# Optimization experiments

Measured on AMD Instinct MI355X. Metric: run time of the kernel, lower is better.

Reference implementation:

```python
import jax, jax.numpy as jnp
import numpy as np

N = 131072
IN_A = 256
IN_V = 512
IN_VF = 512
CH = 256
BN_EPS = 1e-5
COS_EPS = 1e-8


def setup_inputs() -> dict:
    key = jax.random.key(0)
    ks = jax.random.split(key, 12)
    s = 0.05
    return {
        "x": jax.random.normal(ks[0], (N, 4, 512), dtype=jnp.float32),
        "audio_node_mask": jax.random.bernoulli(ks[1], 0.5, (N,)),
        "W_a": jax.random.normal(ks[2], (IN_A, CH), dtype=jnp.float32) * s,
        "b_a": jnp.zeros((CH,), jnp.float32),
        "W_v": jax.random.normal(ks[3], (IN_V, CH), dtype=jnp.float32) * s,
        "b_v": jnp.zeros((CH,), jnp.float32),
        "W_f": jax.random.normal(ks[4], (2 * CH, CH), dtype=jnp.float32) * s,
        "b_f": jnp.zeros((CH,), jnp.float32),
        "gamma": jnp.ones((CH,), jnp.float32),
        "beta": jnp.zeros((CH,), jnp.float32),
        "W_fc": jax.random.normal(ks[5], (CH, 2), dtype=jnp.float32) * s,
        "b_fc": jnp.zeros((2,), jnp.float32),
    }


def reference(x, audio_node_mask, W_a, b_a, W_v, b_v, W_f, b_f, gamma, beta, W_fc, b_fc):
    # Slice per-type features (x: [N, 4, 512])
    a_in = x[:, 0, :IN_A]    # audio feats (also video->audio feats)
    v_in = x[:, 1, :IN_V]    # video feats
    a_vf = x[:, 2, :IN_VF]   # audio voice-face emb
    v_vf = x[:, 3, :IN_VF]   # video voice-face emb

    # cosine similarity along feature dim (torch.nn.functional.cosine_similarity semantics)
    dot = jnp.sum(a_vf * v_vf, axis=1)
    denom = jnp.maximum(jnp.linalg.norm(a_vf, axis=1) * jnp.linalg.norm(v_vf, axis=1), COS_EPS)
    sim = dot / denom  # [N]

    # per-type linears (compute densely, select by mask -> same math as masked scatter)
    a_out = a_in @ W_a + b_a                                   # [N, CH]
    v_out = v_in @ W_v + b_v                                   # [N, CH]
    va = a_in * sim[:, None]                                   # sim-weighted audio feats on video nodes
    fused = jnp.concatenate([va, v_out], axis=1) @ W_f + b_f   # [N, CH]

    graph_feats = jnp.where(audio_node_mask[:, None], a_out, fused)

    # BatchNorm1d (training: batch statistics, biased variance)
    mu = jnp.mean(graph_feats, axis=0)
    var = jnp.mean(jnp.square(graph_feats - mu), axis=0)
    graph_feats = (graph_feats - mu) * jax.lax.rsqrt(var + BN_EPS) * gamma + beta

    graph_feats = jax.nn.relu(graph_feats)
    return graph_feats @ W_fc + b_fc  # [N, 2]
```

## Files before the change

### kernel.cpp

```cpp
#include <hip/hip_runtime.h>
#include <hip/hip_bf16.h>
#include <stdint.h>

#define NN 131072

typedef unsigned int uint;
typedef unsigned short ushort;
typedef __attribute__((ext_vector_type(8))) __bf16 bf16x8;
typedef __attribute__((ext_vector_type(2))) __bf16 bf16x2;
typedef __attribute__((ext_vector_type(4))) float f32x4;


__device__ __forceinline__ ushort f2bf(float f) {
    uint u = __float_as_uint(f);
    u += 0x7FFF + ((u >> 16) & 1);
    return (ushort)(u >> 16);
}
__device__ __forceinline__ uint pk2(float a, float b) {
    bf16x2 t;
    t[0] = (__bf16)a;
    t[1] = (__bf16)b;
    return __builtin_bit_cast(uint, t);
}
__device__ __forceinline__ bool mask_val(const unsigned char* m8, int flag, int i) {
    return flag ? (m8[(size_t)i * 4] != 0) : (m8[i] != 0);
}
__device__ __forceinline__ size_t pack_off(int k, int c) {
    return (size_t)(((k >> 5) * 16 + (c >> 4)) * 512
                    + (((k >> 3) & 3) * 16 + (c & 15)) * 8 + (k & 7));
}

__global__ void k_detect(const uint* m32, int n, int* flag) {
    __shared__ int cnt;
    if (threadIdx.x == 0) cnt = 0;
    __syncthreads();
    int local = 0;
    int nw = n >> 2;
    for (int i = threadIdx.x; i < nw; i += 1024)
        if (m32[i] & 0x0000FF00u) local = 1;
    if (local) atomicAdd(&cnt, 1);
    __syncthreads();
    if (threadIdx.x == 0) *flag = (cnt == 0) ? 1 : 0;
}

__global__ void k_count(const unsigned char* m8, const int* flagp, int* cntM) {
    int flag = *flagp;
    int t = threadIdx.x;
    bool m = mask_val(m8, flag, blockIdx.x * 256 + t);
    unsigned long long bal = __ballot(m);
    __shared__ int wsum[4];
    if ((t & 63) == 0) wsum[t >> 6] = __popcll(bal);
    __syncthreads();
    if (t == 0) cntM[blockIdx.x] = wsum[0] + wsum[1] + wsum[2] + wsum[3];
}

__global__ void k_scan(const int* __restrict__ cntM, int* __restrict__ meta,
                       int* __restrict__ baseA, int* __restrict__ baseF) {
    __shared__ int sA[512], sF[512];
    int t = threadIdx.x;
    int a = cntM[t], f = 256 - a;
    sA[t] = a; sF[t] = f;
    __syncthreads();
    for (int off = 1; off < 512; off <<= 1) {
        int va = (t >= off) ? sA[t - off] : 0;
        int vf = (t >= off) ? sF[t - off] : 0;
        __syncthreads();
        sA[t] += va; sF[t] += vf;
        __syncthreads();
    }
    baseA[t] = sA[t] - a;
    baseF[t] = sF[t] - f;
    if (t == 511) { meta[2] = sA[511]; meta[1] = sF[511]; }
}

__global__ void k_fill(const unsigned char* m8, const int* flagp,
                       const int* __restrict__ baseA, const int* __restrict__ baseF,
                       int* __restrict__ audioIdx, int* __restrict__ fusedIdx) {
    int flag = *flagp;
    int blk = blockIdx.x, t = threadIdx.x;
    int row = blk * 256 + t;
    bool m = mask_val(m8, flag, row);
    unsigned long long bal = __ballot(m);
    int lane = t & 63, w = t >> 6;
    unsigned long long lt = (1ull << lane) - 1ull;
    int pA = __popcll(bal & lt);
    __shared__ int wA[4];
    if (lane == 0) wA[w] = __popcll(bal);
    __syncthreads();
    int offA = 0;
    for (int i = 0; i < w; ++i) offA += wA[i];
    int offF = w * 64 - offA;
    int pF = lane - pA;
    if (m) audioIdx[baseA[blk] + offA + pA] = row;
    else   fusedIdx[baseF[blk] + offF + pF] = row;
}

__global__ void k_prep(const float* __restrict__ Wa, const float* __restrict__ Wf,
                       const float* __restrict__ Wv, const float* __restrict__ bv,
                       const float* __restrict__ bf_, ushort* __restrict__ Bwa,
                       ushort* __restrict__ Bwf, float* __restrict__ cf) {
    int c = threadIdx.x;
    int b = blockIdx.x;
    if (b < 256) {
        Bwa[pack_off(b, c)] = f2bf(Wa[b * 256 + c]);
    } else if (b < 512) {
        Bwf[pack_off(512 + (b - 256), c)] = f2bf(Wf[(b - 256) * 256 + c]);
    } else if (b < 1024) {
        int k = b - 512;
        const float* wr = Wv + k * 256;
        float acc = 0.f;
        for (int j = 0; j < 256; ++j) acc += wr[j] * Wf[(256 + j) * 256 + c];
        Bwf[pack_off(k, c)] = f2bf(acc);
    } else {
        float acc = bf_[c];
        for (int j = 0; j < 256; ++j) acc += bv[j] * Wf[(256 + j) * 256 + c];
        cf[c] = acc;
    }
}

__global__ __launch_bounds__(512, 4) void k_main(
    const float* __restrict__ x, const int* __restrict__ meta,
    const int* __restrict__ fusedIdx, const int* __restrict__ audioIdx,
    const ushort* __restrict__ Bwa, const ushort* __restrict__ Bwf,
    const float* __restrict__ ba, const float* __restrict__ cf,
    ushort* __restrict__ gf, float* __restrict__ bn_s, float* __restrict__ bn_q)
{
    __shared__ bf16x8 As8[2][128 * 8];
    __shared__ int ridxS[128];
    __shared__ float simS[128];
    __shared__ unsigned char validS[128];
    __shared__ float redS[256], redQ[256];

    const int tid = threadIdx.x;
    const int cntF = meta[1], cntA = meta[2];
    const int nbF = (cntF + 127) >> 7;
    const int nbA = (cntA + 127) >> 7;
    const int b = blockIdx.x;
    const bool isF = b < nbF;
    const int bb = isF ? b : b - nbF;

    if (!isF && bb >= nbA) {
        if (tid < 256) {
            bn_s[(size_t)b * 256 + tid] = 0.f;
            bn_q[(size_t)b * 256 + tid] = 0.f;
        }
        return;
    }

    const int cnt = isF ? cntF : cntA;
    const int* idxArr = isF ? fusedIdx : audioIdx;
    const int lane = tid & 63;
    const int w = tid >> 6, wr = w >> 2, wc = w & 3;
    const int fr = lane & 15, fg = lane >> 4;

    if (tid < 128) {
        int gpos = bb * 128 + tid;
        int ok = gpos < cnt;
        ridxS[tid] = ok ? idxArr[gpos] : 0;
        validS[tid] = ok;
        simS[tid] = 1.f;
    }
    __syncthreads();

    const int NS = isF ? 12 : 4;
    const int sr = tid >> 2, sk = tid & 3;
    const float* xrow = x + (size_t)ridxS[sr] * 2048;
    const float sVf = validS[sr] ? 1.f : 0.f;
    float sAf = 0.f;

    int4 pA[2];
    auto loadA = [&](int st) {
        const float scl = (isF && st >= 8) ? sAf : sVf;
        const int off = isF ? ((st < 8) ? 512 + st * 64 : (st - 8) * 64) : st * 64;
        const float4* src = (const float4*)(xrow + off + sk * 16);
        #pragma unroll
        for (int s = 0; s < 2; ++s) {
            float4 u0 = src[2 * s], u1 = src[2 * s + 1];
            int4 p;
            p.x = pk2(u0.x * scl, u0.y * scl);
            p.y = pk2(u0.z * scl, u0.w * scl);
            p.z = pk2(u1.x * scl, u1.y * scl);
            p.w = pk2(u1.z * scl, u1.w * scl);
            pA[s] = p;
        }
    };
    auto storeA = [&](int buf) {
        #pragma unroll
        for (int s = 0; s < 2; ++s)
            As8[buf][sr * 8 + ((sk * 2 + s) ^ (sr & 7))] = __builtin_bit_cast(bf16x8, pA[s]);
    };

    loadA(0);

    if (isF) {
        #pragma unroll 2
        for (int rr = 0; rr < 16; ++rr) {
            int r = w * 16 + rr;
            const float4* p = (const float4*)(x + (size_t)ridxS[r] * 2048 + 1024);
            float4 a0 = p[lane], a1 = p[lane + 64];
            float4 v0 = p[lane + 128], v1 = p[lane + 192];
            float dot = a0.x * v0.x + a0.y * v0.y + a0.z * v0.z + a0.w * v0.w
                      + a1.x * v1.x + a1.y * v1.y + a1.z * v1.z + a1.w * v1.w;
            float na = a0.x * a0.x + a0.y * a0.y + a0.z * a0.z + a0.w * a0.w
                     + a1.x * a1.x + a1.y * a1.y + a1.z * a1.z + a1.w * a1.w;
            float nv = v0.x * v0.x + v0.y * v0.y + v0.z * v0.z + v0.w * v0.w
                     + v1.x * v1.x + v1.y * v1.y + v1.z * v1.z + v1.w * v1.w;
            #pragma unroll
            for (int off = 32; off; off >>= 1) {
                dot += __shfl_xor(dot, off);
                na  += __shfl_xor(na,  off);
                nv  += __shfl_xor(nv,  off);
            }
            if (lane == 0)
                simS[r] = dot / fmaxf(sqrtf(na) * sqrtf(nv), 1e-8f);
        }
    }
    __syncthreads();
    sAf = validS[sr] ? simS[sr] : 0.f;

    const ushort* bBase = (isF ? Bwf : Bwa) + ((size_t)(wc * 4) << 9) + (lane << 3);

    f32x4 acc[4][4];
    #pragma unroll
    for (int m = 0; m < 4; ++m)
        #pragma unroll
        for (int n = 0; n < 4; ++n) acc[m][n] = (f32x4){0.f, 0.f, 0.f, 0.f};

    storeA(0);
    __syncthreads();

    for (int st = 0; st < NS; ++st) {
        if (st + 1 < NS) loadA(st + 1);
        const int buf = st & 1;
        #pragma unroll
        for (int kk = 0; kk < 2; ++kk) {
            bf16x8 bv[4], af[4];
            #pragma unroll
            for (int n = 0; n < 4; ++n)
                bv[n] = *(const bf16x8*)(bBase + ((size_t)((st * 2 + kk) * 16 + n) << 9));
            #pragma unroll
            for (int m = 0; m < 4; ++m) {
                int r = wr * 64 + m * 16 + fr;
                af[m] = As8[buf][r * 8 + ((kk * 4 + fg) ^ (r & 7))];
            }
            #pragma unroll
            for (int n = 0; n < 4; ++n)
                #pragma unroll
                for (int m = 0; m < 4; ++m)
                    acc[m][n] = __builtin_amdgcn_mfma_f32_16x16x32_bf16(
                        af[m], bv[n], acc[m][n], 0, 0, 0);
        }
        if (st + 1 < NS) storeA((st + 1) & 1);
        __syncthreads();
    }

    if (tid < 256) { redS[tid] = 0.f; redQ[tid] = 0.f; }
    __syncthreads();

    const int colLo = wc * 64 + fr;
    const float* biasp = isF ? cf : ba;
    float bN[4];
    #pragma unroll
    for (int n = 0; n < 4; ++n) bN[n] = biasp[colLo + n * 16];

    float cs[4] = {0.f, 0.f, 0.f, 0.f}, cq[4] = {0.f, 0.f, 0.f, 0.f};
    #pragma unroll
    for (int m = 0; m < 4; ++m) {
        #pragma unroll
        for (int j = 0; j < 4; ++j) {
            int rloc = wr * 64 + m * 16 + fg * 4 + j;
            if (!validS[rloc]) continue;
            ushort* grow = gf + (size_t)ridxS[rloc] * 256;
            #pragma unroll
            for (int n = 0; n < 4; ++n) {
                float g = acc[m][n][j] + bN[n];
                grow[colLo + n * 16] = f2bf(g);
                cs[n] += g;
                cq[n] += g * g;
            }
        }
    }
    #pragma unroll
    for (int n = 0; n < 4; ++n) {
        atomicAdd(&redS[colLo + n * 16], cs[n]);
        atomicAdd(&redQ[colLo + n * 16], cq[n]);
    }
    __syncthreads();
    if (tid < 256) {
        bn_s[(size_t)b * 256 + tid] = redS[tid];
        bn_q[(size_t)b * 256 + tid] = redQ[tid];
    }
}

__global__ void k_stats(const float* __restrict__ bn_s, const float* __restrict__ bn_q,
                        const float* __restrict__ gamma, const float* __restrict__ beta,
                        float* __restrict__ scale, float* __restrict__ shift) {
    int c = blockIdx.x;
    int t = threadIdx.x;
    float s = 0.f, q = 0.f;
    for (int r = t; r < 1025; r += 256) {
        s += bn_s[(size_t)r * 256 + c];
        q += bn_q[(size_t)r * 256 + c];
    }
    __shared__ float ss[256], qq[256];
    ss[t] = s; qq[t] = q;
    __syncthreads();
    for (int off = 128; off; off >>= 1) {
        if (t < off) { ss[t] += ss[t + off]; qq[t] += qq[t + off]; }
        __syncthreads();
    }
    if (t == 0) {
        float mu  = ss[0] / 131072.f;
        float var = qq[0] / 131072.f - mu * mu;
        float sc = gamma[c] * rsqrtf(var + 1e-5f);
        scale[c] = sc;
        shift[c] = beta[c] - mu * sc;
    }
}

__global__ void k_out(const ushort* __restrict__ gf, const float* __restrict__ scale,
                      const float* __restrict__ shift, const float* __restrict__ Wfc,
                      const float* __restrict__ bfc, float* __restrict__ out) {
    int wid = threadIdx.x >> 6;
    int lane = threadIdx.x & 63;
    int i = blockIdx.x * 4 + wid;
    uint2 gv = ((const uint2*)(gf + (size_t)i * 256))[lane];
    float g0 = __uint_as_float(gv.x << 16);
    float g1 = __uint_as_float(gv.x & 0xFFFF0000u);
    float g2 = __uint_as_float(gv.y << 16);
    float g3 = __uint_as_float(gv.y & 0xFFFF0000u);
    int c0 = lane * 4;
    float4 sc = *(const float4*)(scale + c0);
    float4 sh = *(const float4*)(shift + c0);
    float y0 = fmaxf(g0 * sc.x + sh.x, 0.f);
    float y1 = fmaxf(g1 * sc.y + sh.y, 0.f);
    float y2 = fmaxf(g2 * sc.z + sh.z, 0.f);
    float y3 = fmaxf(g3 * sc.w + sh.w, 0.f);
    const float4* w = (const float4*)(Wfc + c0 * 2);
    float4 w0 = w[0], w1 = w[1];
    float p0 = y0 * w0.x + y1 * w0.z + y2 * w1.x + y3 * w1.z;
    float p1 = y0 * w0.y + y1 * w0.w + y2 * w1.y + y3 * w1.w;
    #pragma unroll
    for (int off = 32; off; off >>= 1) {
        p0 += __shfl_xor(p0, off);
        p1 += __shfl_xor(p1, off);
    }
    if (lane == 0) {
        out[(size_t)i * 2]     = p0 + bfc[0];
        out[(size_t)i * 2 + 1] = p1 + bfc[1];
    }
}

extern "C" void kernel_launch(void* const* d_in, const int* in_sizes, int n_in,
                              void* d_out, int out_size, void* d_ws, size_t ws_size,
                              hipStream_t stream) {
    const float* x          = (const float*)d_in[0];
    const unsigned char* mk = (const unsigned char*)d_in[1];
    const float* Wa  = (const float*)d_in[2];
    const float* ba  = (const float*)d_in[3];
    const float* Wv  = (const float*)d_in[4];
    const float* bv  = (const float*)d_in[5];
    const float* Wf  = (const float*)d_in[6];
    const float* bf  = (const float*)d_in[7];
    const float* gamma = (const float*)d_in[8];
    const float* beta  = (const float*)d_in[9];
    const float* Wfc = (const float*)d_in[10];
    const float* bfc = (const float*)d_in[11];
    float* out = (float*)d_out;

    char* ws = (char*)d_ws;
    int*    meta   = (int*)ws;
    float*  scale  = (float*)(ws + 1024);
    float*  shift  = (float*)(ws + 2048);
    float*  cf     = (float*)(ws + 3072);
    int*    cntM   = (int*)(ws + 8192);
    int*    baseA  = (int*)(ws + 12288);
    int*    baseF  = (int*)(ws + 16384);
    ushort* Bwa    = (ushort*)(ws + 32768);
    ushort* Bwf    = (ushort*)(ws + 262144);
    int*    fusedIdx = (int*)(ws + (1u << 20));
    int*    audioIdx = (int*)(ws + (1u << 20) + (512u << 10));
    float*  bn_s   = (float*)(ws + (2u << 20));
    float*  bn_q   = (float*)(ws + (4u << 20));
    ushort* gf     = (ushort*)(ws + (8u << 20));

    int n = in_sizes[1];

    k_detect<<<1, 1024, 0, stream>>>((const uint*)mk, n, meta);
    k_count<<<512, 256, 0, stream>>>(mk, meta, cntM);
    k_scan<<<1, 512, 0, stream>>>(cntM, meta, baseA, baseF);
    k_fill<<<512, 256, 0, stream>>>(mk, meta, baseA, baseF, audioIdx, fusedIdx);
    k_prep<<<1025, 256, 0, stream>>>(Wa, Wf, Wv, bv, bf, Bwa, Bwf, cf);
    k_main<<<1025, 512, 0, stream>>>(x, meta, fusedIdx, audioIdx, Bwa, Bwf, ba, cf,
                                     gf, bn_s, bn_q);
    k_stats<<<256, 256, 0, stream>>>(bn_s, bn_q, gamma, beta, scale, shift);
    k_out<<<NN / 4, 256, 0, stream>>>(gf, scale, shift, Wfc, bfc, out);
}
```

Before: 244.3 us.

## Shrink main GEMM tile to 32 rows with full-K LDS panel staging

The main fused GEMM kernel now processes 32 gathered rows per block instead of 128. Each block loads the full-K bf16 A panel into LDS once, computing cosine similarity in the same pass with nontemporal loads, then runs the MFMA loop with no per-stage syncs or double buffering. This raises block count about fourfold for better latency hiding and parallelism, at the cost of reloading the weight B tiles once per 32 rows and a larger BN partial-sum reduction. The mask detect kernel is also vectorized and the prep loops are unrolled.

```diff
diff --git a/kernel.cpp b/kernel.cpp
--- a/kernel.cpp
+++ b/kernel.cpp
@@ -11,6 +11,8 @@
 typedef __attribute__((ext_vector_type(4))) float f32x4;
 
 
+#define NB_MAIN 4098
+
 __device__ __forceinline__ ushort f2bf(float f) {
     uint u = __float_as_uint(f);
     u += 0x7FFF + ((u >> 16) & 1);
@@ -30,21 +32,24 @@
                     + (((k >> 3) & 3) * 16 + (c & 15)) * 8 + (k & 7));
 }
 
-__global__ void k_detect(const uint* m32, int n, int* flag) {
+__global__ void k_detect(const uint4* m128, int n, int* cntNZ) {
     __shared__ int cnt;
     if (threadIdx.x == 0) cnt = 0;
     __syncthreads();
     int local = 0;
-    int nw = n >> 2;
-    for (int i = threadIdx.x; i < nw; i += 1024)
-        if (m32[i] & 0x0000FF00u) local = 1;
+    int nv = n >> 4;
+    #pragma unroll 4
+    for (int i = threadIdx.x; i < nv; i += 256) {
+        uint4 v = m128[i];
+        if ((v.x | v.y | v.z | v.w) & 0x0000FF00u) local = 1;
+    }
     if (local) atomicAdd(&cnt, 1);
     __syncthreads();
-    if (threadIdx.x == 0) *flag = (cnt == 0) ? 1 : 0;
-}
-
-__global__ void k_count(const unsigned char* m8, const int* flagp, int* cntM) {
-    int flag = *flagp;
+    if (threadIdx.x == 0) *cntNZ = cnt;
+}
+
+__global__ void k_count(const unsigned char* m8, const int* cntNZp, int* cntM) {
+    int flag = (*cntNZp == 0) ? 1 : 0;
     int t = threadIdx.x;
     bool m = mask_val(m8, flag, blockIdx.x * 256 + t);
     unsigned long long bal = __ballot(m);
@@ -73,10 +78,10 @@
     if (t == 511) { meta[2] = sA[511]; meta[1] = sF[511]; }
 }
 
-__global__ void k_fill(const unsigned char* m8, const int* flagp,
+__global__ void k_fill(const unsigned char* m8, const int* cntNZp,
                        const int* __restrict__ baseA, const int* __restrict__ baseF,
                        int* __restrict__ audioIdx, int* __restrict__ fusedIdx) {
-    int flag = *flagp;
+    int flag = (*cntNZp == 0) ? 1 : 0;
     int blk = blockIdx.x, t = threadIdx.x;
     int row = blk * 256 + t;
     bool m = mask_val(m8, flag, row);
@@ -109,10 +114,12 @@
         int k = b - 512;
         const float* wr = Wv + k * 256;
         float acc = 0.f;
+        #pragma unroll 8
         for (int j = 0; j < 256; ++j) acc += wr[j] * Wf[(256 + j) * 256 + c];
         Bwf[pack_off(k, c)] = f2bf(acc);
     } else {
         float acc = bf_[c];
+        #pragma unroll 8
         for (int j = 0; j < 256; ++j) acc += bv[j] * Wf[(256 + j) * 256 + c];
         cf[c] = acc;
     }
@@ -125,16 +132,15 @@
     const float* __restrict__ ba, const float* __restrict__ cf,
     ushort* __restrict__ gf, float* __restrict__ bn_s, float* __restrict__ bn_q)
 {
-    __shared__ bf16x8 As8[2][128 * 8];
-    __shared__ int ridxS[128];
-    __shared__ float simS[128];
-    __shared__ unsigned char validS[128];
+    __shared__ ushort panel[32 * 768];
+    __shared__ int ridxS[32];
+    __shared__ unsigned char validS[32];
     __shared__ float redS[256], redQ[256];
 
     const int tid = threadIdx.x;
     const int cntF = meta[1], cntA = meta[2];
-    const int nbF = (cntF + 127) >> 7;
-    const int nbA = (cntA + 127) >> 7;
+    const int nbF = (cntF + 31) >> 5;
+    const int nbA = (cntA + 31) >> 5;
     const int b = blockIdx.x;
     const bool isF = b < nbF;
     const int bb = isF ? b : b - nbF;
@@ -153,109 +159,83 @@
     const int w = tid >> 6, wr = w >> 2, wc = w & 3;
     const int fr = lane & 15, fg = lane >> 4;
 
-    if (tid < 128) {
-        int gpos = bb * 128 + tid;
+    if (tid < 32) {
+        int gpos = bb * 32 + tid;
         int ok = gpos < cnt;
         ridxS[tid] = ok ? idxArr[gpos] : 0;
         validS[tid] = ok;
-        simS[tid] = 1.f;
+    }
+    if (tid < 256) { redS[tid] = 0.f; redQ[tid] = 0.f; }
+    __syncthreads();
+
+    {
+        const int sw = lane >> 1;
+        const int o4 = (lane & 1) * 4;
+        #pragma unroll 2
+        for (int rr = 0; rr < 4; ++rr) {
+            int r = w * 4 + rr;
+            const f32x4* bp = (const f32x4*)(x + (size_t)ridxS[r] * 2048);
+            float sv = validS[r] ? 1.f : 0.f;
+            ushort* prow = panel + r * 768;
+            int rx = r & 7;
+            if (isF) {
+                f32x4 ta = __builtin_nontemporal_load(bp + lane);
+                f32x4 t0 = __builtin_nontemporal_load(bp + 128 + lane);
+                f32x4 t1 = __builtin_nontemporal_load(bp + 192 + lane);
+                f32x4 t2 = __builtin_nontemporal_load(bp + 256 + lane);
+                f32x4 t3 = __builtin_nontemporal_load(bp + 320 + lane);
+                f32x4 t4 = __builtin_nontemporal_load(bp + 384 + lane);
+                f32x4 t5 = __builtin_nontemporal_load(bp + 448 + lane);
+                float dot = t2.x * t4.x + t2.y * t4.y + t2.z * t4.z + t2.w * t4.w
+                          + t3.x * t5.x + t3.y * t5.y + t3.z * t5.z + t3.w * t5.w;
+                float na = t2.x * t2.x + t2.y * t2.y + t2.z * t2.z + t2.w * t2.w
+                         + t3.x * t3.x + t3.y * t3.y + t3.z * t3.z + t3.w * t3.w;
+                float nv = t4.x * t4.x + t4.y * t4.y + t4.z * t4.z + t4.w * t4.w
+                         + t5.x * t5.x + t5.y * t5.y + t5.z * t5.z + t5.w * t5.w;
+                #pragma unroll
+                for (int off = 32; off; off >>= 1) {
+                    dot += __shfl_xor(dot, off);
+                    na  += __shfl_xor(na,  off);
+                    nv  += __shfl_xor(nv,  off);
+                }
+                float sim = dot / fmaxf(sqrtf(na * nv), 1e-8f);
+                float sa = sv * sim;
+                uint2 q0 = {pk2(t0.x * sv, t0.y * sv), pk2(t0.z * sv, t0.w * sv)};
+                uint2 q1 = {pk2(t1.x * sv, t1.y * sv), pk2(t1.z * sv, t1.w * sv)};
+                uint2 qa = {pk2(ta.x * sa, ta.y * sa), pk2(ta.z * sa, ta.w * sa)};
+                *(uint2*)(prow + ((sw ^ rx) << 3) + o4)          = q0;
+                *(uint2*)(prow + (((32 + sw) ^ rx) << 3) + o4)   = q1;
+                *(uint2*)(prow + (((64 + sw) ^ rx) << 3) + o4)   = qa;
+            } else {
+                f32x4 ta = __builtin_nontemporal_load(bp + lane);
+                uint2 qa = {pk2(ta.x * sv, ta.y * sv), pk2(ta.z * sv, ta.w * sv)};
+                *(uint2*)(prow + ((sw ^ rx) << 3) + o4) = qa;
+            }
+        }
     }
     __syncthreads();
 
     const int NS = isF ? 12 : 4;
-    const int sr = tid >> 2, sk = tid & 3;
-    const float* xrow = x + (size_t)ridxS[sr] * 2048;
-    const float sVf = validS[sr] ? 1.f : 0.f;
-    float sAf = 0.f;
-
-    int4 pA[2];
-    auto loadA = [&](int st) {
-        const float scl = (isF && st >= 8) ? sAf : sVf;
-        const int off = isF ? ((st < 8) ? 512 + st * 64 : (st - 8) * 64) : st * 64;
-        const float4* src = (const float4*)(xrow + off + sk * 16);
-        #pragma unroll
-        for (int s = 0; s < 2; ++s) {
-            float4 u0 = src[2 * s], u1 = src[2 * s + 1];
-            int4 p;
-            p.x = pk2(u0.x * scl, u0.y * scl);
-            p.y = pk2(u0.z * scl, u0.w * scl);
-            p.z = pk2(u1.x * scl, u1.y * scl);
-            p.w = pk2(u1.z * scl, u1.w * scl);
-            pA[s] = p;
-        }
-    };
-    auto storeA = [&](int buf) {
-        #pragma unroll
-        for (int s = 0; s < 2; ++s)
-            As8[buf][sr * 8 + ((sk * 2 + s) ^ (sr & 7))] = __builtin_bit_cast(bf16x8, pA[s]);
-    };
-
-    loadA(0);
-
-    if (isF) {
-        #pragma unroll 2
-        for (int rr = 0; rr < 16; ++rr) {
-            int r = w * 16 + rr;
-            const float4* p = (const float4*)(x + (size_t)ridxS[r] * 2048 + 1024);
-            float4 a0 = p[lane], a1 = p[lane + 64];
-            float4 v0 = p[lane + 128], v1 = p[lane + 192];
-            float dot = a0.x * v0.x + a0.y * v0.y + a0.z * v0.z + a0.w * v0.w
-                      + a1.x * v1.x + a1.y * v1.y + a1.z * v1.z + a1.w * v1.w;
-            float na = a0.x * a0.x + a0.y * a0.y + a0.z * a0.z + a0.w * a0.w
-                     + a1.x * a1.x + a1.y * a1.y + a1.z * a1.z + a1.w * a1.w;
-            float nv = v0.x * v0.x + v0.y * v0.y + v0.z * v0.z + v0.w * v0.w
-                     + v1.x * v1.x + v1.y * v1.y + v1.z * v1.z + v1.w * v1.w;
-            #pragma unroll
-            for (int off = 32; off; off >>= 1) {
-                dot += __shfl_xor(dot, off);
-                na  += __shfl_xor(na,  off);
-                nv  += __shfl_xor(nv,  off);
-            }
-            if (lane == 0)
-                simS[r] = dot / fmaxf(sqrtf(na) * sqrtf(nv), 1e-8f);
-        }
-    }
-    __syncthreads();
-    sAf = validS[sr] ? simS[sr] : 0.f;
-
     const ushort* bBase = (isF ? Bwf : Bwa) + ((size_t)(wc * 4) << 9) + (lane << 3);
-
-    f32x4 acc[4][4];
-    #pragma unroll
-    for (int m = 0; m < 4; ++m)
-        #pragma unroll
-        for (int n = 0; n < 4; ++n) acc[m][n] = (f32x4){0.f, 0.f, 0.f, 0.f};
-
-    storeA(0);
-    __syncthreads();
+    const int rrd = wr * 16 + fr;
+    const ushort* prd = panel + rrd * 768;
+    const int rxr = rrd & 7;
+
+    f32x4 acc[4];
+    #pragma unroll
+    for (int n = 0; n < 4; ++n) acc[n] = (f32x4){0.f, 0.f, 0.f, 0.f};
 
     for (int st = 0; st < NS; ++st) {
-        if (st + 1 < NS) loadA(st + 1);
-        const int buf = st & 1;
         #pragma unroll
         for (int kk = 0; kk < 2; ++kk) {
-            bf16x8 bv[4], af[4];
+            bf16x8 af = *(const bf16x8*)(prd + (((st * 8 + kk * 4 + fg) ^ rxr) << 3));
             #pragma unroll
-            for (int n = 0; n < 4; ++n)
-                bv[n] = *(const bf16x8*)(bBase + ((size_t)((st * 2 + kk) * 16 + n) << 9));
-            #pragma unroll
-            for (int m = 0; m < 4; ++m) {
-                int r = wr * 64 + m * 16 + fr;
-                af[m] = As8[buf][r * 8 + ((kk * 4 + fg) ^ (r & 7))];
+            for (int n = 0; n < 4; ++n) {
+                bf16x8 bv = *(const bf16x8*)(bBase + ((size_t)((st * 2 + kk) * 16 + n) << 9));
+                acc[n] = __builtin_amdgcn_mfma_f32_16x16x32_bf16(af, bv, acc[n], 0, 0, 0);
             }
-            #pragma unroll
-            for (int n = 0; n < 4; ++n)
-                #pragma unroll
-                for (int m = 0; m < 4; ++m)
-                    acc[m][n] = __builtin_amdgcn_mfma_f32_16x16x32_bf16(
-                        af[m], bv[n], acc[m][n], 0, 0, 0);
         }
-        if (st + 1 < NS) storeA((st + 1) & 1);
-        __syncthreads();
-    }
-
-    if (tid < 256) { redS[tid] = 0.f; redQ[tid] = 0.f; }
-    __syncthreads();
+    }
 
     const int colLo = wc * 64 + fr;
     const float* biasp = isF ? cf : ba;
@@ -265,15 +245,13 @@
 
     float cs[4] = {0.f, 0.f, 0.f, 0.f}, cq[4] = {0.f, 0.f, 0.f, 0.f};
     #pragma unroll
-    for (int m = 0; m < 4; ++m) {
-        #pragma unroll
-        for (int j = 0; j < 4; ++j) {
-            int rloc = wr * 64 + m * 16 + fg * 4 + j;
-            if (!validS[rloc]) continue;
+    for (int j = 0; j < 4; ++j) {
+        int rloc = wr * 16 + fg * 4 + j;
+        if (validS[rloc]) {
             ushort* grow = gf + (size_t)ridxS[rloc] * 256;
             #pragma unroll
             for (int n = 0; n < 4; ++n) {
-                float g = acc[m][n][j] + bN[n];
+                float g = acc[n][j] + bN[n];
                 grow[colLo + n * 16] = f2bf(g);
                 cs[n] += g;
                 cq[n] += g * g;
@@ -298,7 +276,7 @@
     int c = blockIdx.x;
     int t = threadIdx.x;
     float s = 0.f, q = 0.f;
-    for (int r = t; r < 1025; r += 256) {
+    for (int r = t; r < NB_MAIN; r += 256) {
         s += bn_s[(size_t)r * 256 + c];
         q += bn_q[(size_t)r * 256 + c];
     }
@@ -380,19 +358,19 @@
     ushort* Bwf    = (ushort*)(ws + 262144);
     int*    fusedIdx = (int*)(ws + (1u << 20));
     int*    audioIdx = (int*)(ws + (1u << 20) + (512u << 10));
-    float*  bn_s   = (float*)(ws + (2u << 20));
-    float*  bn_q   = (float*)(ws + (4u << 20));
-    ushort* gf     = (ushort*)(ws + (8u << 20));
+    float*  bn_s   = (float*)(ws + (8u << 20));
+    float*  bn_q   = (float*)(ws + (16u << 20));
+    ushort* gf     = (ushort*)(ws + (32u << 20));
 
     int n = in_sizes[1];
 
-    k_detect<<<1, 1024, 0, stream>>>((const uint*)mk, n, meta);
+    k_detect<<<1, 256, 0, stream>>>((const uint4*)mk, n, meta);
     k_count<<<512, 256, 0, stream>>>(mk, meta, cntM);
     k_scan<<<1, 512, 0, stream>>>(cntM, meta, baseA, baseF);
     k_fill<<<512, 256, 0, stream>>>(mk, meta, baseA, baseF, audioIdx, fusedIdx);
     k_prep<<<1025, 256, 0, stream>>>(Wa, Wf, Wv, bv, bf, Bwa, Bwf, cf);
-    k_main<<<1025, 512, 0, stream>>>(x, meta, fusedIdx, audioIdx, Bwa, Bwf, ba, cf,
-                                     gf, bn_s, bn_q);
+    k_main<<<NB_MAIN, 512, 0, stream>>>(x, meta, fusedIdx, audioIdx, Bwa, Bwf, ba, cf,
+                                        gf, bn_s, bn_q);
     k_stats<<<256, 256, 0, stream>>>(bn_s, bn_q, gamma, beta, scale, shift);
     k_out<<<NN / 4, 256, 0, stream>>>(gf, scale, shift, Wfc, bfc, out);
 }
```

Result: slower. 284.9 us (+16.6%).
